# Kernel optimization log

Measured on AMD Instinct MI355X. Metric: run time of the kernel, lower is better.

Reference implementation:

```python
import jax, jax.numpy as jnp
import numpy as np

N_NODES = 100_000
N_EDGES = 3_200_000
WEIGHT_LIMIT = 5000.0
RIDGE = 1e-7


def _polynomial_basis(diff):
    # diff: [E, 2] -> [E, 5] basis (x, y, x*y, x^2, y^2)
    x = diff[:, 0]
    y = diff[:, 1]
    return jnp.stack([x, y, x * y, x * x, y * y], axis=-1)


def setup_inputs() -> dict:
    key = jax.random.key(0)
    k1, k2, k3 = jax.random.split(key, 3)
    pos = jax.random.normal(k1, (N_NODES, 2), dtype=jnp.float32)
    row = jax.random.randint(k2, (N_EDGES,), 0, N_NODES, dtype=jnp.int64)
    col = jax.random.randint(k3, (N_EDGES,), 0, N_NODES, dtype=jnp.int64)
    edge_index = jnp.stack([row, col], axis=0)
    return {"pos": pos, "edge_index": edge_index}


def reference(pos, edge_index):
    # With a dense random graph, 2-hop extension adds no edges, so the
    # augmented edge_index equals the original edge_index.
    row = edge_index[0]
    col = edge_index[1]
    n = pos.shape[0]

    # Edge displacement (detached in the original module).
    diff = jax.lax.stop_gradient(pos[col] - pos[row])  # [E, 2]
    H = _polynomial_basis(diff).astype(jnp.float32)    # [E, 5]

    # Per-edge outer products, scatter-accumulated per source node.
    M_edge = H[:, :, None] * H[:, None, :]                          # [E, 5, 5]
    M_node = jax.ops.segment_sum(M_edge, row, num_segments=n)      # [N, 5, 5]
    M_node = M_node + RIDGE * jnp.eye(5, dtype=jnp.float32)

    # Laplacian RHS: [0, 0, 0, 2, 2] per node (coefficients of x^2, y^2).
    L = jnp.zeros((n, 5), dtype=jnp.float32).at[:, 3:].set(2.0)

    # C = M^{-1} L (per-node 5x5 solve).
    C = jnp.linalg.solve(M_node, L[..., None])[..., 0]              # [N, 5]

    # Per-edge Laplacian weights.
    weights = jnp.sum(C[row] * H, axis=1)                           # [E]
    return jnp.clip(weights, -WEIGHT_LIMIT, WEIGHT_LIMIT)
```

## Files before the change

kernel.cpp:

```cpp
#include <hip/hip_runtime.h>
#include <math.h>

constexpr float WLIM = 5000.0f;
constexpr double RIDGE = 1e-7;

#define G 256
#define MAXNB 1024
#define BN 128
#define CAP 5120
#define EBUF_CAP 12544

__global__ __launch_bounds__(1024) void k_sort(const int* __restrict__ row,
                                               const int* __restrict__ col,
                                               int* __restrict__ table,
                                               unsigned int* __restrict__ sorted,
                                               unsigned short* __restrict__ posmap,
                                               int nE, int CE, int NB) {
    __shared__ int h[MAXNB];
    __shared__ int wt[16];
    __shared__ unsigned int ebuf[EBUF_CAP];
    const int g = blockIdx.x, tid = threadIdx.x;
    const int lane = tid & 63, wid = tid >> 6;
    const int s = g * CE;
    const int e_end = min(s + CE, nE);
    const int cnt = e_end - s;
    const bool vec = ((CE & 3) == 0);

    for (int i = tid; i < MAXNB; i += 1024) h[i] = 0;
    __syncthreads();
    if (vec) {
        const int4* r4p = (const int4*)(row + s);
        int nv = cnt >> 2;
        for (int i = tid; i < nv; i += 1024) {
            int4 r4 = r4p[i];
            atomicAdd(&h[r4.x >> 7], 1);
            atomicAdd(&h[r4.y >> 7], 1);
            atomicAdd(&h[r4.z >> 7], 1);
            atomicAdd(&h[r4.w >> 7], 1);
        }
        for (int i = (nv << 2) + tid; i < cnt; i += 1024)
            atomicAdd(&h[row[s + i] >> 7], 1);
    } else {
        for (int i = s + tid; i < e_end; i += 1024)
            atomicAdd(&h[row[i] >> 7], 1);
    }
    __syncthreads();
    int v = h[tid];
    int x = v;
    #pragma unroll
    for (int d = 1; d < 64; d <<= 1) {
        int u = __shfl_up(x, d);
        if (lane >= d) x += u;
    }
    if (lane == 63) wt[wid] = x;
    __syncthreads();
    if (tid < 16) {
        int w = wt[tid];
        int xx = w;
        #pragma unroll
        for (int d = 1; d < 16; d <<= 1) {
            int u = __shfl_up(xx, d);
            if (tid >= d) xx += u;
        }
        wt[tid] = xx - w;
    }
    __syncthreads();
    int excl = (x - v) + wt[wid];
    if (tid < NB) {
        table[(size_t)tid * G + g] = excl;
        h[tid] = excl;
    }
    if (tid == 0) table[(size_t)NB * G + g] = cnt;
    __syncthreads();
    if (vec) {
        const int4* r4p = (const int4*)(row + s);
        const int4* c4p = (const int4*)(col + s);
        ushort4* pm4 = (ushort4*)(posmap + s);
        int nv = cnt >> 2;
        for (int i = tid; i < nv; i += 1024) {
            int4 r4 = r4p[i];
            int4 c4 = c4p[i];
            int p0 = atomicAdd(&h[r4.x >> 7], 1); ebuf[p0] = ((unsigned)(r4.x & 127) << 17) | (unsigned)c4.x;
            int p1 = atomicAdd(&h[r4.y >> 7], 1); ebuf[p1] = ((unsigned)(r4.y & 127) << 17) | (unsigned)c4.y;
            int p2 = atomicAdd(&h[r4.z >> 7], 1); ebuf[p2] = ((unsigned)(r4.z & 127) << 17) | (unsigned)c4.z;
            int p3 = atomicAdd(&h[r4.w >> 7], 1); ebuf[p3] = ((unsigned)(r4.w & 127) << 17) | (unsigned)c4.w;
            pm4[i] = make_ushort4((unsigned short)p0, (unsigned short)p1,
                                  (unsigned short)p2, (unsigned short)p3);
        }
        for (int i = (nv << 2) + tid; i < cnt; i += 1024) {
            int r = row[s + i], c = col[s + i];
            int p = atomicAdd(&h[r >> 7], 1);
            ebuf[p] = ((unsigned)(r & 127) << 17) | (unsigned)c;
            posmap[s + i] = (unsigned short)p;
        }
    } else {
        for (int i = tid; i < cnt; i += 1024) {
            int r = row[s + i], c = col[s + i];
            int p = atomicAdd(&h[r >> 7], 1);
            ebuf[p] = ((unsigned)(r & 127) << 17) | (unsigned)c;
            posmap[s + i] = (unsigned short)p;
        }
    }
    __syncthreads();
    if (vec) {
        uint4* dst = (uint4*)(sorted + s);
        const uint4* src = (const uint4*)ebuf;
        int nv = cnt >> 2;
        for (int i = tid; i < nv; i += 1024) dst[i] = src[i];
        for (int i = (nv << 2) + tid; i < cnt; i += 1024) sorted[s + i] = ebuf[i];
    } else {
        for (int i = tid; i < cnt; i += 1024) sorted[s + i] = ebuf[i];
    }
}

__global__ __launch_bounds__(256) void k_node3(const float2* __restrict__ pos,
                                               unsigned int* __restrict__ sorted,
                                               const int* __restrict__ table,
                                               int nN, int CE, int NB) {
    __shared__ unsigned int ebuf[CAP];
    __shared__ int cnt[BN];
    __shared__ int off[BN + 1];
    __shared__ int cur[BN];
    __shared__ int goff0[G], glen[G];
    __shared__ int wt2[2];
    __shared__ float crec[BN * 8];
    const int b = blockIdx.x, tid = threadIdx.x;

    int off0 = table[(size_t)b * G + tid];
    int off1 = table[(size_t)(b + 1) * G + tid];
    int len = off1 - off0;
    goff0[tid] = off0; glen[tid] = len;
    if (tid < BN) cnt[tid] = 0;
    __syncthreads();

    const int gbase = tid * CE + off0;
    for (int j = 0; j < len; ++j)
        atomicAdd(&cnt[sorted[gbase + j] >> 17], 1);
    __syncthreads();
    int sv = 0, sx = 0;
    if (tid < BN) {
        sv = cnt[tid];
        sx = sv;
        #pragma unroll
        for (int d = 1; d < 64; d <<= 1) {
            int u = __shfl_up(sx, d);
            if ((tid & 63) >= d) sx += u;
        }
        if ((tid & 63) == 63) wt2[tid >> 6] = sx;
    }
    __syncthreads();
    if (tid < BN) {
        int incl = sx + ((tid >> 6) ? wt2[0] : 0);
        off[tid] = incl - sv;
        cur[tid] = incl - sv;
        if (tid == BN - 1) off[BN] = incl;
    }
    __syncthreads();
    const int total = off[BN];

    const bool fits = (total <= CAP);
    if (fits) {
        for (int j = 0; j < len; ++j) {
            unsigned v = sorted[gbase + j];
            int p = atomicAdd(&cur[(int)(v >> 17)], 1);
            ebuf[p] = v & 0x1FFFFu;
        }
    }
    __syncthreads();

    const int node = tid >> 1;
    const int half = tid & 1;
    const int n = (b << 7) + node;
    float m[15];
    #pragma unroll
    for (int i = 0; i < 15; ++i) m[i] = 0.0f;
    float2 pr = make_float2(0.f, 0.f);
    if (n < nN) {
        pr = pos[n];
        if (fits) {
            int j0 = off[node], j1 = off[node + 1];
            for (int j = j0 + half; j < j1; j += 2) {
                float2 pc = pos[ebuf[j]];
                float x = pc.x - pr.x;
                float y = pc.y - pr.y;
                float xy = x * y, xx = x * x, yy = y * y;
                m[0]  += x * x;   m[1]  += x * y;   m[2]  += x * xy;  m[3]  += x * xx;  m[4]  += x * yy;
                m[5]  += y * y;   m[6]  += y * xy;  m[7]  += y * xx;  m[8]  += y * yy;
                m[9]  += xy * xy; m[10] += xy * xx; m[11] += xy * yy;
                m[12] += xx * xx; m[13] += xx * yy;
                m[14] += yy * yy;
            }
        } else {
            for (int g2 = half; g2 < G; g2 += 2) {
                int base2 = g2 * CE + goff0[g2];
                for (int j = 0; j < glen[g2]; ++j) {
                    unsigned v = sorted[base2 + j];
                    if ((int)(v >> 17) == node) {
                        float2 pc = pos[v & 0x1FFFFu];
                        float x = pc.x - pr.x;
                        float y = pc.y - pr.y;
                        float xy = x * y, xx = x * x, yy = y * y;
                        m[0]  += x * x;   m[1]  += x * y;   m[2]  += x * xy;  m[3]  += x * xx;  m[4]  += x * yy;
                        m[5]  += y * y;   m[6]  += y * xy;  m[7]  += y * xx;  m[8]  += y * yy;
                        m[9]  += xy * xy; m[10] += xy * xx; m[11] += xy * yy;
                        m[12] += xx * xx; m[13] += xx * yy;
                        m[14] += yy * yy;
                    }
                }
            }
        }
    }
    #pragma unroll
    for (int i = 0; i < 15; ++i) m[i] += __shfl_xor(m[i], 1);

    if (half == 0 && n < nN) {
        double A[5][5];
        {
            int idx = 0;
            #pragma unroll
            for (int i = 0; i < 5; ++i) {
                #pragma unroll
                for (int j = i; j < 5; ++j) {
                    double vv = (double)m[idx++];
                    A[i][j] = vv;
                    A[j][i] = vv;
                }
            }
        }
        #pragma unroll
        for (int i = 0; i < 5; ++i) A[i][i] += RIDGE;

        #pragma unroll
        for (int k = 0; k < 5; ++k) {
            double d = A[k][k];
            d = sqrt(fmax(d, 1e-300));
            A[k][k] = d;
            double inv = 1.0 / d;
            #pragma unroll
            for (int i = k + 1; i < 5; ++i) A[i][k] *= inv;
            #pragma unroll
            for (int j = k + 1; j < 5; ++j) {
                #pragma unroll
                for (int i = j; i < 5; ++i) A[i][j] -= A[i][k] * A[j][k];
            }
        }
        double bb[5] = {0.0, 0.0, 0.0, 2.0, 2.0};
        double y[5];
        #pragma unroll
        for (int i = 0; i < 5; ++i) {
            double sv2 = bb[i];
            #pragma unroll
            for (int k = 0; k < 5; ++k) {
                if (k < i) sv2 -= A[i][k] * y[k];
            }
            y[i] = sv2 / A[i][i];
        }
        double xs[5];
        #pragma unroll
        for (int ii = 4; ii >= 0; --ii) {
            double sv2 = y[ii];
            #pragma unroll
            for (int k = 0; k < 5; ++k) {
                if (k > ii) sv2 -= A[k][ii] * xs[k];
            }
            xs[ii] = sv2 / A[ii][ii];
        }
        float* cb = &crec[node * 8];
        #pragma unroll
        for (int i = 0; i < 5; ++i) cb[i] = (float)xs[i];
        cb[5] = pr.x;
        cb[6] = pr.y;
    }
    __syncthreads();

    float* wout = (float*)sorted;
    for (int j = 0; j < len; ++j) {
        unsigned v = sorted[gbase + j];
        int lr = (int)(v >> 17);
        int c = (int)(v & 0x1FFFFu);
        const float* cb = &crec[lr * 8];
        float2 pc = pos[c];
        float x = pc.x - cb[5];
        float y = pc.y - cb[6];
        float w = cb[0] * x + cb[1] * y + cb[2] * (x * y) + cb[3] * (x * x) + cb[4] * (y * y);
        w = fminf(fmaxf(w, -WLIM), WLIM);
        wout[gbase + j] = w;
    }
}

__global__ __launch_bounds__(1024) void k_unsort(const float* __restrict__ wsorted,
                                                 const unsigned short* __restrict__ posmap,
                                                 float* __restrict__ out, int nE, int CE) {
    __shared__ float wl[EBUF_CAP];
    const int g = blockIdx.x, tid = threadIdx.x;
    const int s = g * CE;
    const int e_end = min(s + CE, nE);
    const int cnt = e_end - s;
    const bool vec = ((CE & 3) == 0);
    if (vec) {
        const uint4* src = (const uint4*)(wsorted + s);
        uint4* dstl = (uint4*)wl;
        int nv = cnt >> 2;
        for (int i = tid; i < nv; i += 1024) dstl[i] = src[i];
        for (int i = (nv << 2) + tid; i < cnt; i += 1024) wl[i] = wsorted[s + i];
        __syncthreads();
        const ushort4* pm4 = (const ushort4*)(posmap + s);
        float4* out4 = (float4*)(out + s);
        for (int i = tid; i < nv; i += 1024) {
            ushort4 p4 = pm4[i];
            float4 o;
            o.x = wl[p4.x]; o.y = wl[p4.y]; o.z = wl[p4.z]; o.w = wl[p4.w];
            out4[i] = o;
        }
        for (int i = (nv << 2) + tid; i < cnt; i += 1024) out[s + i] = wl[posmap[s + i]];
    } else {
        for (int i = tid; i < cnt; i += 1024) wl[i] = wsorted[s + i];
        __syncthreads();
        for (int i = tid; i < cnt; i += 1024) out[s + i] = wl[posmap[s + i]];
    }
}

extern "C" void kernel_launch(void* const* d_in, const int* in_sizes, int n_in,
                              void* d_out, int out_size, void* d_ws, size_t ws_size,
                              hipStream_t stream) {
    const float2* pos = (const float2*)d_in[0];
    const int* ei = (const int*)d_in[1];
    const int nN = in_sizes[0] / 2;
    const int nE = in_sizes[1] / 2;
    const int* row = ei;
    const int* col = ei + nE;

    const int NB = (nN + BN - 1) >> 7;
    const int CE = (nE + G - 1) / G;

    int* table = (int*)d_ws;
    size_t poff_ints = (((size_t)(NB + 1) * G) + 1) & ~(size_t)1;
    unsigned short* posmap = (unsigned short*)((int*)d_ws + poff_ints);

    unsigned int* sorted = (unsigned int*)d_out;
    float* out = (float*)d_out;

    k_sort<<<G, 1024, 0, stream>>>(row, col, table, sorted, posmap, nE, CE, NB);
    k_node3<<<NB, 256, 0, stream>>>(pos, sorted, table, nN, CE, NB);
    k_unsort<<<G, 1024, 0, stream>>>((const float*)sorted, posmap, out, nE, CE);
}
```

Baseline: 90.08 us.

## Split per-node solve and per-edge weight pass into separate kernels

The node kernel now writes its solved 5-coefficient vectors to a global workspace array instead of shared memory and returns. A new kernel reloads those coefficients plus node positions into a smaller shared tile and computes the per-edge weights. This separates the heavy double-precision solve from the memory-bound edge pass, aiming for better occupancy and lower shared-memory and register pressure in each part. The cost is an extra launch, a global round-trip for coefficients, and re-reading the sorted edge list and offset table.

```diff
diff --git a/kernel.cpp b/kernel.cpp
--- a/kernel.cpp
+++ b/kernel.cpp
@@ -114,8 +114,9 @@
 }
 
 __global__ __launch_bounds__(256) void k_node3(const float2* __restrict__ pos,
-                                               unsigned int* __restrict__ sorted,
+                                               const unsigned int* __restrict__ sorted,
                                                const int* __restrict__ table,
+                                               float* __restrict__ rec,
                                                int nN, int CE, int NB) {
     __shared__ unsigned int ebuf[CAP];
     __shared__ int cnt[BN];
@@ -123,7 +124,6 @@
     __shared__ int cur[BN];
     __shared__ int goff0[G], glen[G];
     __shared__ int wt2[2];
-    __shared__ float crec[BN * 8];
     const int b = blockIdx.x, tid = threadIdx.x;
 
     int off0 = table[(size_t)b * G + tid];
@@ -265,20 +265,41 @@
             }
             xs[ii] = sv2 / A[ii][ii];
         }
-        float* cb = &crec[node * 8];
+        float* cb = rec + (size_t)n * 5;
         #pragma unroll
         for (int i = 0; i < 5; ++i) cb[i] = (float)xs[i];
-        cb[5] = pr.x;
-        cb[6] = pr.y;
-    }
-    __syncthreads();
-
+    }
+}
+
+__global__ __launch_bounds__(256) void k_wsorted(const float2* __restrict__ pos,
+                                                 unsigned int* __restrict__ sorted,
+                                                 const int* __restrict__ table,
+                                                 const float* __restrict__ rec,
+                                                 int nN, int CE, int NB) {
+    __shared__ float crec[BN * 7];
+    const int b = blockIdx.x, tid = threadIdx.x;
+    for (int i = tid; i < BN * 5; i += 256) {
+        int node = i / 5, k = i - node * 5;
+        crec[node * 7 + k] = rec[(size_t)(b << 7) * 5 + i];
+    }
+    if (tid < BN) {
+        int n = (b << 7) + tid;
+        float2 p = (n < nN) ? pos[n] : make_float2(0.f, 0.f);
+        crec[tid * 7 + 5] = p.x;
+        crec[tid * 7 + 6] = p.y;
+    }
+    __syncthreads();
+
+    int off0 = table[(size_t)b * G + tid];
+    int off1 = table[(size_t)(b + 1) * G + tid];
+    int len = off1 - off0;
+    const int gbase = tid * CE + off0;
     float* wout = (float*)sorted;
     for (int j = 0; j < len; ++j) {
         unsigned v = sorted[gbase + j];
         int lr = (int)(v >> 17);
         int c = (int)(v & 0x1FFFFu);
-        const float* cb = &crec[lr * 8];
+        const float* cb = &crec[lr * 7];
         float2 pc = pos[c];
         float x = pc.x - cb[5];
         float y = pc.y - cb[6];
@@ -334,13 +355,15 @@
     const int CE = (nE + G - 1) / G;
 
     int* table = (int*)d_ws;
-    size_t poff_ints = (((size_t)(NB + 1) * G) + 1) & ~(size_t)1;
-    unsigned short* posmap = (unsigned short*)((int*)d_ws + poff_ints);
+    float* rec = (float*)(table + (size_t)(NB + 1) * G);
+    size_t pm_off_ints = ((size_t)(NB + 1) * G + (size_t)NB * BN * 5 + 1) & ~(size_t)1;
+    unsigned short* posmap = (unsigned short*)((int*)d_ws + pm_off_ints);
 
     unsigned int* sorted = (unsigned int*)d_out;
     float* out = (float*)d_out;
 
     k_sort<<<G, 1024, 0, stream>>>(row, col, table, sorted, posmap, nE, CE, NB);
-    k_node3<<<NB, 256, 0, stream>>>(pos, sorted, table, nN, CE, NB);
+    k_node3<<<NB, 256, 0, stream>>>(pos, sorted, table, rec, nN, CE, NB);
+    k_wsorted<<<NB, 256, 0, stream>>>(pos, sorted, table, rec, nN, CE, NB);
     k_unsort<<<G, 1024, 0, stream>>>((const float*)sorted, posmap, out, nE, CE);
 }
```

Result: slower. 98.69 us (+9.6%).
